# Performance work log

Hardware: AMD Instinct MI355X
Metric: run time of the kernel (lower is better)

The kernel has to match this reference:

```python
import jax, jax.numpy as jnp
import numpy as np

N_BLADES = 8

def _build_cayley():
    """Geometric-product table for Cl(3,0): C[i,j,k] s.t. (e_i * e_j) = sum_k C[i,j,k] e_k.
    Blade order: [1, e1, e2, e3, e12, e13, e23, e123] via bitmasks [0,1,2,4,3,5,6,7]."""
    blades = [0, 1, 2, 4, 3, 5, 6, 7]
    idx = {b: i for i, b in enumerate(blades)}
    C = np.zeros((8, 8, 8), dtype=np.float32)
    for i, a in enumerate(blades):
        for j, b in enumerate(blades):
            aa = a >> 1
            cnt = 0
            while aa:
                cnt += bin(aa & b).count('1')
                aa >>= 1
            sign = -1.0 if (cnt & 1) else 1.0
            C[i, j, idx[a ^ b]] += sign
    return jnp.asarray(C)

CAYLEY = _build_cayley()

def clifford_linear(x, w, b):
    # x: (..., 8), w: (8,), b: (8,) -> geometric product w * x + b
    return jnp.einsum('ijk,i,...j->...k', CAYLEY, w, x) + b

def setup_inputs() -> dict:
    key = jax.random.key(0)
    ks = jax.random.split(key, 9)
    B, S = 4, 4096
    inp = {'x': jax.random.normal(ks[0], (B, S, N_BLADES), dtype=jnp.float32)}
    names = ['wq', 'bq', 'wk', 'bk', 'wv', 'bv', 'wo', 'bo']
    for i, n in enumerate(names):
        scale = 1.0 / np.sqrt(N_BLADES) if n.startswith('w') else 0.02
        inp[n] = jax.random.normal(ks[i + 1], (N_BLADES,), dtype=jnp.float32) * scale
    return inp

def reference(x, wq, bq, wk, bk, wv, bv, wo, bo):
    # head_dim = max(1, 8 // 2) = 4 -> scale = sqrt(4) = 2
    scale = jnp.float32(2.0)
    Q = clifford_linear(x, wq, bq)  # (B,S,8)
    K = clifford_linear(x, wk, bk)
    V = clifford_linear(x, wv, bv)
    c0 = CAYLEY[..., 0]  # (8,8) scalar part of geometric product
    attn = jnp.einsum('ij,bsi,btj->bst', c0, Q, K) / scale  # (B,S,S)
    attn = jax.nn.softmax(attn, axis=-1)
    out = jnp.einsum('bst,btk->bsk', attn, V)  # (B,S,8)
    return clifford_linear(out, wo, bo)
```

## Files before the change

kernel.cpp:

```cpp
#include <hip/hip_runtime.h>
#include <math.h>

#define SEQ 4096
#define NBATCH 4
#define SGRP 32
#define TWAVES 8
#define TCHUNK (SEQ / TWAVES)
#define TT 32
#define VTILE 288

typedef _Float16 f16;
typedef __attribute__((ext_vector_type(8))) _Float16 f16x8;
typedef __attribute__((ext_vector_type(8))) __bf16 bf16x8;
typedef __attribute__((ext_vector_type(16))) float f32x16;
typedef __attribute__((ext_vector_type(4))) unsigned u32x4;
typedef __attribute__((ext_vector_type(2))) unsigned u32x2;

__device__ __forceinline__ float fexp2(float x) {
#if __has_builtin(__builtin_amdgcn_exp2f)
  return __builtin_amdgcn_exp2f(x);
#else
  return exp2f(x);
#endif
}

__device__ __forceinline__ u32x2 pswap(unsigned a, unsigned b) {
#if __has_builtin(__builtin_amdgcn_permlane32_swap)
  return __builtin_amdgcn_permlane32_swap(a, b, false, false);
#else
  asm volatile("v_permlane32_swap_b32 %0, %1" : "+v"(a), "+v"(b));
  u32x2 r; r[0] = a; r[1] = b; return r;
#endif
}

__device__ __forceinline__ unsigned exp2_pk_bf16(float a, float b) {
  unsigned e0 = __builtin_bit_cast(unsigned, fexp2(a));
  unsigned e1 = __builtin_bit_cast(unsigned, fexp2(b));
  return __builtin_amdgcn_perm(e1, e0, 0x07060302u);
}

__device__ __forceinline__ unsigned short f2bf(float f) {
  unsigned u = __builtin_bit_cast(unsigned, f);
  u += 0x7FFF + ((u >> 16) & 1);
  return (unsigned short)(u >> 16);
}

__device__ __forceinline__ float cl_sign(int amask, int bmask) {
  int cnt = 0, aa = amask >> 1;
  while (aa) { cnt += __popc(aa & bmask); aa >>= 1; }
  return (cnt & 1) ? -1.f : 1.f;
}

__global__ __launch_bounds__(128) void ck_qkv(const float* __restrict__ x,
                                              const float* __restrict__ wq,
                                              const float* __restrict__ bq,
                                              const float* __restrict__ wk,
                                              const float* __restrict__ bk,
                                              const float* __restrict__ wv,
                                              const float* __restrict__ bv,
                                              f16* __restrict__ Qp,
                                              f16* __restrict__ Kp,
                                              unsigned short* __restrict__ Vt) {
  __shared__ float Pl[288];
  const int blades[8] = {0, 1, 2, 4, 3, 5, 6, 7};
  int tid = threadIdx.x;

  if (tid < 64) {
    int j = tid >> 3, k = tid & 7;
    int bj = blades[j];
    float mq = 0.f, mk = 0.f, mv = 0.f;
    for (int i = 0; i < 8; ++i) {
      int ai = blades[i];
      if (blades[ai ^ bj] != k) continue;
      float sgn = cl_sign(ai, bj);
      mq += sgn * wq[i]; mk += sgn * wk[i]; mv += sgn * wv[i];
    }
    float c0 = cl_sign(blades[k], blades[k]);
    const float F = 0.72134752044448170368f;
    Pl[tid]       = mq * c0 * F;
    Pl[64 + tid]  = mk;
    Pl[128 + tid] = mv;
    if (j == 0) {
      Pl[256 + k] = bq[k] * c0 * F;
      Pl[264 + k] = bk[k];
      Pl[272 + k] = bv[k];
    }
  }
  __syncthreads();

  int row = blockIdx.x * 128 + tid;
  int b = row >> 12;
  int s = row & (SEQ - 1);
  const float4* x4 = (const float4*)(x + (size_t)row * 8);
  float4 xa = x4[0], xb = x4[1];
  float xr[8] = {xa.x, xa.y, xa.z, xa.w, xb.x, xb.y, xb.z, xb.w};
  float q[8], k[8], v[8];
#pragma unroll
  for (int c = 0; c < 8; ++c) { q[c] = Pl[256 + c]; k[c] = Pl[264 + c]; v[c] = Pl[272 + c]; }
#pragma unroll
  for (int j = 0; j < 8; ++j) {
    float xj = xr[j];
#pragma unroll
    for (int c = 0; c < 8; ++c) {
      q[c] = fmaf(xj, Pl[j * 8 + c], q[c]);
      k[c] = fmaf(xj, Pl[64 + j * 8 + c], k[c]);
      v[c] = fmaf(xj, Pl[128 + j * 8 + c], v[c]);
    }
  }
  f16x8 qa, qb, ka;
#pragma unroll
  for (int c = 0; c < 8; ++c) {
    f16 h = (f16)q[c];
    qa[c] = h;
    qb[c] = (f16)(q[c] - (float)h);
    ka[c] = (f16)k[c];
  }
  f16x8* qrow = (f16x8*)(Qp + (size_t)row * 16);
  qrow[0] = qa; qrow[1] = qb;
  *(f16x8*)(Kp + (size_t)row * 8) = ka;
  unsigned short* vt = Vt + ((size_t)b * (SEQ / 32) + (s >> 5)) * VTILE + (s & 31);
#pragma unroll
  for (int c = 0; c < 8; ++c) vt[c * 32] = f2bf(v[c]);
  vt[8 * 32] = 0x3F80;
}

__global__ __launch_bounds__(512, 4) void ck_attn(const f16* __restrict__ Qp,
                                                  const f16* __restrict__ Kp,
                                                  const unsigned short* __restrict__ Vt,
                                                  const float* __restrict__ wo,
                                                  const float* __restrict__ bo,
                                                  float* __restrict__ out) {
  __shared__ float Lo[TWAVES][SGRP][9];
  __shared__ float MoL[72];

  const int tid = threadIdx.x;
  const int w = tid >> 6;
  const int lane = tid & 63;
  const int ls = lane & 31;
  const int hf = lane >> 5;
  const int rowbase = blockIdx.x * SGRP;
  const int b = rowbase >> 12;

  if (tid < 64) {
    const int blades[8] = {0, 1, 2, 4, 3, 5, 6, 7};
    int j = tid >> 3, k = tid & 7;
    int bj = blades[j];
    float mo = 0.f;
    for (int i = 0; i < 8; ++i) {
      int ai = blades[i];
      if (blades[ai ^ bj] != k) continue;
      mo += cl_sign(ai, bj) * wo[i];
    }
    MoL[tid] = mo;
    if (j == 0) MoL[64 + k] = bo[k];
  }

  f16x8 qf = *(const f16x8*)(Qp + (size_t)(rowbase + ls) * 16 + 8 * hf);

  f32x16 acc = {0.f, 0.f, 0.f, 0.f, 0.f, 0.f, 0.f, 0.f,
                0.f, 0.f, 0.f, 0.f, 0.f, 0.f, 0.f, 0.f};
  const f32x16 zero = acc;

  const f16* kbase = Kp + ((size_t)b * SEQ + w * TCHUNK + ls) * 8;
  const unsigned short* vbase =
      Vt + ((size_t)b * (SEQ / 32) + w * (TCHUNK / 32)) * VTILE +
      (ls <= 8 ? ls : 8) * 32 + 8 * hf;

  const int NIT = TCHUNK / TT;

#pragma unroll 1
  for (int it = 0; it < NIT; it += 2) {
    const int t0 = it * TT;
    f16x8 kfA = *(const f16x8*)(kbase + (size_t)t0 * 8);
    f16x8 kfB = *(const f16x8*)(kbase + (size_t)(t0 + TT) * 8);
    u32x4 vA0 = *(const u32x4*)(vbase + (size_t)it * VTILE);
    u32x4 vA1 = *(const u32x4*)(vbase + (size_t)it * VTILE + 16);
    u32x4 vB0 = *(const u32x4*)(vbase + (size_t)(it + 1) * VTILE);
    u32x4 vB1 = *(const u32x4*)(vbase + (size_t)(it + 1) * VTILE + 16);

    f32x16 sA = __builtin_amdgcn_mfma_f32_32x32x16_f16(kfA, qf, zero, 0, 0, 0);
    f32x16 sB = __builtin_amdgcn_mfma_f32_32x32x16_f16(kfB, qf, zero, 0, 0, 0);

    {
      unsigned d0 = exp2_pk_bf16(sA[0], sA[1]);
      unsigned d1 = exp2_pk_bf16(sA[2], sA[3]);
      unsigned d2 = exp2_pk_bf16(sA[4], sA[5]);
      unsigned d3 = exp2_pk_bf16(sA[6], sA[7]);
      u32x2 r02 = pswap(d0, d2);
      u32x2 r13 = pswap(d1, d3);
      u32x4 pb0 = {r02[0], r13[0], r02[1], r13[1]};
      acc = __builtin_amdgcn_mfma_f32_32x32x16_bf16(
          __builtin_bit_cast(bf16x8, vA0), __builtin_bit_cast(bf16x8, pb0), acc, 0, 0, 0);
      unsigned d4 = exp2_pk_bf16(sA[8], sA[9]);
      unsigned d5 = exp2_pk_bf16(sA[10], sA[11]);
      unsigned d6 = exp2_pk_bf16(sA[12], sA[13]);
      unsigned d7 = exp2_pk_bf16(sA[14], sA[15]);
      u32x2 r46 = pswap(d4, d6);
      u32x2 r57 = pswap(d5, d7);
      u32x4 pb1 = {r46[0], r57[0], r46[1], r57[1]};
      acc = __builtin_amdgcn_mfma_f32_32x32x16_bf16(
          __builtin_bit_cast(bf16x8, vA1), __builtin_bit_cast(bf16x8, pb1), acc, 0, 0, 0);
    }
    {
      unsigned d0 = exp2_pk_bf16(sB[0], sB[1]);
      unsigned d1 = exp2_pk_bf16(sB[2], sB[3]);
      unsigned d2 = exp2_pk_bf16(sB[4], sB[5]);
      unsigned d3 = exp2_pk_bf16(sB[6], sB[7]);
      u32x2 r02 = pswap(d0, d2);
      u32x2 r13 = pswap(d1, d3);
      u32x4 pb0 = {r02[0], r13[0], r02[1], r13[1]};
      acc = __builtin_amdgcn_mfma_f32_32x32x16_bf16(
          __builtin_bit_cast(bf16x8, vB0), __builtin_bit_cast(bf16x8, pb0), acc, 0, 0, 0);
      unsigned d4 = exp2_pk_bf16(sB[8], sB[9]);
      unsigned d5 = exp2_pk_bf16(sB[10], sB[11]);
      unsigned d6 = exp2_pk_bf16(sB[12], sB[13]);
      unsigned d7 = exp2_pk_bf16(sB[14], sB[15]);
      u32x2 r46 = pswap(d4, d6);
      u32x2 r57 = pswap(d5, d7);
      u32x4 pb1 = {r46[0], r57[0], r46[1], r57[1]};
      acc = __builtin_amdgcn_mfma_f32_32x32x16_bf16(
          __builtin_bit_cast(bf16x8, vB1), __builtin_bit_cast(bf16x8, pb1), acc, 0, 0, 0);
    }
  }

  if (hf == 0) {
    Lo[w][ls][0] = acc[0]; Lo[w][ls][1] = acc[1];
    Lo[w][ls][2] = acc[2]; Lo[w][ls][3] = acc[3];
    Lo[w][ls][8] = acc[4];
  } else {
    Lo[w][ls][4] = acc[0]; Lo[w][ls][5] = acc[1];
    Lo[w][ls][6] = acc[2]; Lo[w][ls][7] = acc[3];
  }
  __syncthreads();

  if (tid < SGRP * 9) {
    int s = tid / 9, j = tid - s * 9;
    float sum = 0.f;
#pragma unroll
    for (int w2 = 0; w2 < TWAVES; ++w2) sum += Lo[w2][s][j];
    Lo[0][s][j] = sum;
  }
  __syncthreads();

  if (tid < SGRP * 8) {
    int s = tid >> 3, ko = tid & 7;
    float inv = 1.f / Lo[0][s][8];
    float a = MoL[64 + ko];
#pragma unroll
    for (int j = 0; j < 8; ++j) a = fmaf(Lo[0][s][j] * inv, MoL[j * 8 + ko], a);
    out[(size_t)(rowbase + s) * 8 + ko] = a;
  }
}

extern "C" void kernel_launch(void* const* d_in, const int* in_sizes, int n_in,
                              void* d_out, int out_size, void* d_ws, size_t ws_size,
                              hipStream_t stream) {
  const float* x  = (const float*)d_in[0];
  const float* wq = (const float*)d_in[1];
  const float* bq = (const float*)d_in[2];
  const float* wk = (const float*)d_in[3];
  const float* bk = (const float*)d_in[4];
  const float* wv = (const float*)d_in[5];
  const float* bv = (const float*)d_in[6];
  const float* wo = (const float*)d_in[7];
  const float* bo = (const float*)d_in[8];

  f16* Qp = (f16*)d_ws;
  f16* Kp = Qp + (size_t)NBATCH * SEQ * 16;
  unsigned short* Vt = (unsigned short*)(Kp + (size_t)NBATCH * SEQ * 8);
  float* outp = (float*)d_out;

  hipLaunchKernelGGL(ck_qkv, dim3(NBATCH * SEQ / 128), dim3(128), 0, stream,
                     x, wq, bq, wk, bk, wv, bv, Qp, Kp, Vt);
  hipLaunchKernelGGL(ck_attn, dim3(NBATCH * SEQ / SGRP), dim3(512), 0, stream,
                     Qp, Kp, Vt, wo, bo, outp);
}
```

Before: 21.97 us.

## Process two 32-row query tiles per wave to share K/V loads

Each block now covers 64 query rows with 16 waves and 1024 threads. Each wave keeps two query fragments and two accumulators, so one K fragment and one pair of V tiles per iteration feed both query tiles, halving K/V global traffic per unit of work. The loop drops the 2x key-tile unroll, since the two query tiles already give independent MFMA chains. The trade-offs are more live registers per wave and half as many blocks, which cuts scheduling flexibility across CUs, while the total wave count stays the same.

```diff
diff --git a/kernel.cpp b/kernel.cpp
--- a/kernel.cpp
+++ b/kernel.cpp
@@ -3,8 +3,8 @@
 
 #define SEQ 4096
 #define NBATCH 4
-#define SGRP 32
-#define TWAVES 8
+#define SGRP 64
+#define TWAVES 16
 #define TCHUNK (SEQ / TWAVES)
 #define TT 32
 #define VTILE 288
@@ -124,12 +124,12 @@
   vt[8 * 32] = 0x3F80;
 }
 
-__global__ __launch_bounds__(512, 4) void ck_attn(const f16* __restrict__ Qp,
-                                                  const f16* __restrict__ Kp,
-                                                  const unsigned short* __restrict__ Vt,
-                                                  const float* __restrict__ wo,
-                                                  const float* __restrict__ bo,
-                                                  float* __restrict__ out) {
+__global__ __launch_bounds__(1024, 4) void ck_attn(const f16* __restrict__ Qp,
+                                                   const f16* __restrict__ Kp,
+                                                   const unsigned short* __restrict__ Vt,
+                                                   const float* __restrict__ wo,
+                                                   const float* __restrict__ bo,
+                                                   float* __restrict__ out) {
   __shared__ float Lo[TWAVES][SGRP][9];
   __shared__ float MoL[72];
 
@@ -155,11 +155,13 @@
     if (j == 0) MoL[64 + k] = bo[k];
   }
 
-  f16x8 qf = *(const f16x8*)(Qp + (size_t)(rowbase + ls) * 16 + 8 * hf);
-
-  f32x16 acc = {0.f, 0.f, 0.f, 0.f, 0.f, 0.f, 0.f, 0.f,
-                0.f, 0.f, 0.f, 0.f, 0.f, 0.f, 0.f, 0.f};
-  const f32x16 zero = acc;
+  f16x8 qf0 = *(const f16x8*)(Qp + (size_t)(rowbase + ls) * 16 + 8 * hf);
+  f16x8 qf1 = *(const f16x8*)(Qp + (size_t)(rowbase + 32 + ls) * 16 + 8 * hf);
+
+  f32x16 acc0 = {0.f, 0.f, 0.f, 0.f, 0.f, 0.f, 0.f, 0.f,
+                 0.f, 0.f, 0.f, 0.f, 0.f, 0.f, 0.f, 0.f};
+  f32x16 acc1 = acc0;
+  const f32x16 zero = acc0;
 
   const f16* kbase = Kp + ((size_t)b * SEQ + w * TCHUNK + ls) * 8;
   const unsigned short* vbase =
@@ -169,67 +171,69 @@
   const int NIT = TCHUNK / TT;
 
 #pragma unroll 1
-  for (int it = 0; it < NIT; it += 2) {
+  for (int it = 0; it < NIT; ++it) {
     const int t0 = it * TT;
-    f16x8 kfA = *(const f16x8*)(kbase + (size_t)t0 * 8);
-    f16x8 kfB = *(const f16x8*)(kbase + (size_t)(t0 + TT) * 8);
-    u32x4 vA0 = *(const u32x4*)(vbase + (size_t)it * VTILE);
-    u32x4 vA1 = *(const u32x4*)(vbase + (size_t)it * VTILE + 16);
-    u32x4 vB0 = *(const u32x4*)(vbase + (size_t)(it + 1) * VTILE);
-    u32x4 vB1 = *(const u32x4*)(vbase + (size_t)(it + 1) * VTILE + 16);
-
-    f32x16 sA = __builtin_amdgcn_mfma_f32_32x32x16_f16(kfA, qf, zero, 0, 0, 0);
-    f32x16 sB = __builtin_amdgcn_mfma_f32_32x32x16_f16(kfB, qf, zero, 0, 0, 0);
+    f16x8 kf = *(const f16x8*)(kbase + (size_t)t0 * 8);
+    u32x4 v0 = *(const u32x4*)(vbase + (size_t)it * VTILE);
+    u32x4 v1 = *(const u32x4*)(vbase + (size_t)it * VTILE + 16);
+
+    f32x16 s0 = __builtin_amdgcn_mfma_f32_32x32x16_f16(kf, qf0, zero, 0, 0, 0);
+    f32x16 s1 = __builtin_amdgcn_mfma_f32_32x32x16_f16(kf, qf1, zero, 0, 0, 0);
 
     {
-      unsigned d0 = exp2_pk_bf16(sA[0], sA[1]);
-      unsigned d1 = exp2_pk_bf16(sA[2], sA[3]);
-      unsigned d2 = exp2_pk_bf16(sA[4], sA[5]);
-      unsigned d3 = exp2_pk_bf16(sA[6], sA[7]);
+      unsigned d0 = exp2_pk_bf16(s0[0], s0[1]);
+      unsigned d1 = exp2_pk_bf16(s0[2], s0[3]);
+      unsigned d2 = exp2_pk_bf16(s0[4], s0[5]);
+      unsigned d3 = exp2_pk_bf16(s0[6], s0[7]);
       u32x2 r02 = pswap(d0, d2);
       u32x2 r13 = pswap(d1, d3);
       u32x4 pb0 = {r02[0], r13[0], r02[1], r13[1]};
-      acc = __builtin_amdgcn_mfma_f32_32x32x16_bf16(
-          __builtin_bit_cast(bf16x8, vA0), __builtin_bit_cast(bf16x8, pb0), acc, 0, 0, 0);
-      unsigned d4 = exp2_pk_bf16(sA[8], sA[9]);
-      unsigned d5 = exp2_pk_bf16(sA[10], sA[11]);
-      unsigned d6 = exp2_pk_bf16(sA[12], sA[13]);
-      unsigned d7 = exp2_pk_bf16(sA[14], sA[15]);
+      acc0 = __builtin_amdgcn_mfma_f32_32x32x16_bf16(
+          __builtin_bit_cast(bf16x8, v0), __builtin_bit_cast(bf16x8, pb0), acc0, 0, 0, 0);
+      unsigned d4 = exp2_pk_bf16(s0[8], s0[9]);
+      unsigned d5 = exp2_pk_bf16(s0[10], s0[11]);
+      unsigned d6 = exp2_pk_bf16(s0[12], s0[13]);
+      unsigned d7 = exp2_pk_bf16(s0[14], s0[15]);
       u32x2 r46 = pswap(d4, d6);
       u32x2 r57 = pswap(d5, d7);
       u32x4 pb1 = {r46[0], r57[0], r46[1], r57[1]};
-      acc = __builtin_amdgcn_mfma_f32_32x32x16_bf16(
-          __builtin_bit_cast(bf16x8, vA1), __builtin_bit_cast(bf16x8, pb1), acc, 0, 0, 0);
+      acc0 = __builtin_amdgcn_mfma_f32_32x32x16_bf16(
+          __builtin_bit_cast(bf16x8, v1), __builtin_bit_cast(bf16x8, pb1), acc0, 0, 0, 0);
     }
     {
-      unsigned d0 = exp2_pk_bf16(sB[0], sB[1]);
-      unsigned d1 = exp2_pk_bf16(sB[2], sB[3]);
-      unsigned d2 = exp2_pk_bf16(sB[4], sB[5]);
-      unsigned d3 = exp2_pk_bf16(sB[6], sB[7]);
+      unsigned d0 = exp2_pk_bf16(s1[0], s1[1]);
+      unsigned d1 = exp2_pk_bf16(s1[2], s1[3]);
+      unsigned d2 = exp2_pk_bf16(s1[4], s1[5]);
+      unsigned d3 = exp2_pk_bf16(s1[6], s1[7]);
       u32x2 r02 = pswap(d0, d2);
       u32x2 r13 = pswap(d1, d3);
       u32x4 pb0 = {r02[0], r13[0], r02[1], r13[1]};
-      acc = __builtin_amdgcn_mfma_f32_32x32x16_bf16(
-          __builtin_bit_cast(bf16x8, vB0), __builtin_bit_cast(bf16x8, pb0), acc, 0, 0, 0);
-      unsigned d4 = exp2_pk_bf16(sB[8], sB[9]);
-      unsigned d5 = exp2_pk_bf16(sB[10], sB[11]);
-      unsigned d6 = exp2_pk_bf16(sB[12], sB[13]);
-      unsigned d7 = exp2_pk_bf16(sB[14], sB[15]);
+      acc1 = __builtin_amdgcn_mfma_f32_32x32x16_bf16(
+          __builtin_bit_cast(bf16x8, v0), __builtin_bit_cast(bf16x8, pb0), acc1, 0, 0, 0);
+      unsigned d4 = exp2_pk_bf16(s1[8], s1[9]);
+      unsigned d5 = exp2_pk_bf16(s1[10], s1[11]);
+      unsigned d6 = exp2_pk_bf16(s1[12], s1[13]);
+      unsigned d7 = exp2_pk_bf16(s1[14], s1[15]);
       u32x2 r46 = pswap(d4, d6);
       u32x2 r57 = pswap(d5, d7);
       u32x4 pb1 = {r46[0], r57[0], r46[1], r57[1]};
-      acc = __builtin_amdgcn_mfma_f32_32x32x16_bf16(
-          __builtin_bit_cast(bf16x8, vB1), __builtin_bit_cast(bf16x8, pb1), acc, 0, 0, 0);
+      acc1 = __builtin_amdgcn_mfma_f32_32x32x16_bf16(
+          __builtin_bit_cast(bf16x8, v1), __builtin_bit_cast(bf16x8, pb1), acc1, 0, 0, 0);
     }
   }
 
   if (hf == 0) {
-    Lo[w][ls][0] = acc[0]; Lo[w][ls][1] = acc[1];
-    Lo[w][ls][2] = acc[2]; Lo[w][ls][3] = acc[3];
-    Lo[w][ls][8] = acc[4];
+    Lo[w][ls][0] = acc0[0]; Lo[w][ls][1] = acc0[1];
+    Lo[w][ls][2] = acc0[2]; Lo[w][ls][3] = acc0[3];
+    Lo[w][ls][8] = acc0[4];
+    Lo[w][32 + ls][0] = acc1[0]; Lo[w][32 + ls][1] = acc1[1];
+    Lo[w][32 + ls][2] = acc1[2]; Lo[w][32 + ls][3] = acc1[3];
+    Lo[w][32 + ls][8] = acc1[4];
   } else {
-    Lo[w][ls][4] = acc[0]; Lo[w][ls][5] = acc[1];
-    Lo[w][ls][6] = acc[2]; Lo[w][ls][7] = acc[3];
+    Lo[w][ls][4] = acc0[0]; Lo[w][ls][5] = acc0[1];
+    Lo[w][ls][6] = acc0[2]; Lo[w][ls][7] = acc0[3];
+    Lo[w][32 + ls][4] = acc1[0]; Lo[w][32 + ls][5] = acc1[1];
+    Lo[w][32 + ls][6] = acc1[2]; Lo[w][32 + ls][7] = acc1[3];
   }
   __syncthreads();
 
@@ -272,6 +276,6 @@
 
   hipLaunchKernelGGL(ck_qkv, dim3(NBATCH * SEQ / 128), dim3(128), 0, stream,
                      x, wq, bq, wk, bk, wv, bv, Qp, Kp, Vt);
-  hipLaunchKernelGGL(ck_attn, dim3(NBATCH * SEQ / SGRP), dim3(512), 0, stream,
+  hipLaunchKernelGGL(ck_attn, dim3(NBATCH * SEQ / SGRP), dim3(1024), 0, stream,
                      Qp, Kp, Vt, wo, bo, outp);
 }
```

After: 21.26 us (median of 2 runs). 3.2% less time.
